# Performance work log

Measured on AMD Instinct MI355X. Metric: run time of the kernel, lower is better.

## Reference

```python
import jax, jax.numpy as jnp
import numpy as np

B, G, C = 16384, 7, 30  # batch, 7x7 grid, 2*5 box params + 20 classes


def setup_inputs() -> dict:
    key = jax.random.key(0)
    k1, k2 = jax.random.split(key)
    pred = jax.random.uniform(k1, (B, G, G, C), dtype=jnp.float32)
    labels = jax.random.uniform(k2, (B, G, G, C), dtype=jnp.float32)
    # channel 0 of labels is the object-presence indicator (==1 where a gt box exists)
    labels = labels.at[..., 0].set((labels[..., 0] > 0.7).astype(jnp.float32))
    return {"pred": pred, "labels": labels}


def _corners(box):
    # box channels: [conf, x, y, w, h]
    x, y, w, h = box[..., 1], box[..., 2], box[..., 3], box[..., 4]
    return x - 0.5 * w, x + 0.5 * w, y - 0.5 * h, y + 0.5 * h  # left,right,top,bottom


def _iou(b1, b2):
    l1, r1, t1, bt1 = _corners(b1)
    l2, r2, t2, bt2 = _corners(b2)
    in_h = jnp.minimum(bt1, bt2) - jnp.maximum(t1, t2)
    in_w = jnp.minimum(r1, r2) - jnp.maximum(l1, l2)
    inter = jnp.where((in_h < 0) | (in_w < 0), 0.0, in_h * in_w)
    area1 = (bt1 - t1) * (r1 - l1)
    area2 = (bt2 - t2) * (r2 - l2)
    return inter / (area1 + area2 - inter)


def reference(pred, labels):
    mask = labels[..., 0]                     # [B,7,7] object indicator (0/1)
    box1 = pred[..., 0:5]
    box2 = pred[..., 5:10]
    gt = labels[..., 0:5]
    iou1 = _iou(box1, gt)
    iou2 = _iou(box2, gt)
    best = iou1 >= iou2                       # responsible box per cell
    sel = jnp.where(best[..., None], box1, box2)
    iou_max = jnp.where(best, iou1, iou2)
    iou_min = jnp.where(best, iou2, iou1)
    center = 5.0 * ((sel[..., 1] - gt[..., 1]) ** 2 + (sel[..., 2] - gt[..., 2]) ** 2)
    wh = 5.0 * ((jnp.sqrt(sel[..., 3]) - jnp.sqrt(gt[..., 3])) ** 2
                + (jnp.sqrt(sel[..., 4]) - jnp.sqrt(gt[..., 4])) ** 2)
    cls = jnp.sum((pred[..., 10:] - labels[..., 10:]) ** 2, axis=-1)

    def msum(x):
        return jnp.sum(x * mask)

    # [center, wh, obj_conf, noobj_conf, classification]
    return jnp.stack([msum(center), msum(wh), msum(iou_max), msum(iou_min), msum(cls)])
```

## Files before the change

kernel.cpp:

```cpp
#include <hip/hip_runtime.h>
#include <stdint.h>

#define NCH   30
#define TPB   256
#define TILE  64
#define TW    (TILE * NCH)
#define TF4   (TW / 4)
#define NBLK  2048

__device__ __forceinline__ float iou_f(float x1, float y1, float w1, float h1,
                                       float x2, float y2, float w2, float h2) {
    float l1 = x1 - 0.5f * w1, r1 = x1 + 0.5f * w1;
    float t1 = y1 - 0.5f * h1, b1 = y1 + 0.5f * h1;
    float l2 = x2 - 0.5f * w2, r2 = x2 + 0.5f * w2;
    float t2 = y2 - 0.5f * h2, b2 = y2 + 0.5f * h2;
    float in_h = fminf(b1, b2) - fmaxf(t1, t2);
    float in_w = fminf(r1, r2) - fmaxf(l1, l2);
    float inter = (in_h < 0.f || in_w < 0.f) ? 0.f : in_h * in_w;
    float a1 = (b1 - t1) * (r1 - l1);
    float a2 = (b2 - t2) * (r2 - l2);
    return inter / (a1 + a2 - inter);
}

__device__ __forceinline__ void cell_loss(const float* __restrict__ pp,
                                          const float* __restrict__ lp,
                                          float& v0, float& v1, float& v2,
                                          float& v3, float& v4) {
    const float2 l01 = *(const float2*)(lp);
    const float mask = l01.x;
    if (mask == 0.f) return;

    const float2 l23 = *(const float2*)(lp + 2);
    const float2 l45 = *(const float2*)(lp + 4);
    const float gx = l01.y, gy = l23.x, gw = l23.y, gh = l45.x;

    const float2 p01 = *(const float2*)(pp);
    const float2 p23 = *(const float2*)(pp + 2);
    const float2 p45 = *(const float2*)(pp + 4);
    const float2 p67 = *(const float2*)(pp + 6);
    const float2 p89 = *(const float2*)(pp + 8);

    const float i1 = iou_f(p01.y, p23.x, p23.y, p45.x, gx, gy, gw, gh);
    const float i2 = iou_f(p67.x, p67.y, p89.x, p89.y, gx, gy, gw, gh);
    const bool best = (i1 >= i2);
    const float sx = best ? p01.y : p67.x;
    const float sy = best ? p23.x : p67.y;
    const float sw = best ? p23.y : p89.x;
    const float sh = best ? p45.x : p89.y;
    const float imax = best ? i1 : i2;
    const float imin = best ? i2 : i1;

    const float center = 5.f * ((sx - gx) * (sx - gx) + (sy - gy) * (sy - gy));
    const float dw = sqrtf(sw) - sqrtf(gw);
    const float dh = sqrtf(sh) - sqrtf(gh);
    const float wh = 5.f * (dw * dw + dh * dh);

    float cls = 0.f;
#pragma unroll
    for (int k = 0; k < 10; ++k) {
        const float2 pd = *(const float2*)(pp + 10 + 2 * k);
        const float2 ld = *(const float2*)(lp + 10 + 2 * k);
        const float dx = pd.x - ld.x;
        const float dy = pd.y - ld.y;
        cls += dx * dx + dy * dy;
    }

    v0 += center * mask;
    v1 += wh * mask;
    v2 += imax * mask;
    v3 += imin * mask;
    v4 += cls * mask;
}

__global__ __launch_bounds__(TPB) void yolo_partial(const float* __restrict__ pred,
                                                    const float* __restrict__ lab,
                                                    float* __restrict__ partial,
                                                    int n_cells) {
    __shared__ float s[2 * TW];
    __shared__ float red[5][TPB / 64];

    const int tid  = threadIdx.x;
    const int wave = tid >> 6;
    const int lane = tid & 63;
    const int bid  = blockIdx.x;
    const int NB   = gridDim.x;
    const int nt   = n_cells / TILE;

    float v0 = 0.f, v1 = 0.f, v2 = 0.f, v3 = 0.f, v4 = 0.f;

    const int i0 = tid, i1 = tid + TPB, i2 = tid + 2 * TPB, i3 = tid + 3 * TPB;

    for (int t = bid; t < nt; t += NB) {
        const size_t gbase = (size_t)t * TW;

        {
            const float4* s0 = (const float4*)((i0 < TF4 ? pred + gbase + (size_t)i0 * 4
                                                         : lab  + gbase + (size_t)(i0 - TF4) * 4));
            const float4* s1 = (const float4*)((i1 < TF4 ? pred + gbase + (size_t)i1 * 4
                                                         : lab  + gbase + (size_t)(i1 - TF4) * 4));
            const float4* s2 = (const float4*)((i2 < TF4 ? pred + gbase + (size_t)i2 * 4
                                                         : lab  + gbase + (size_t)(i2 - TF4) * 4));
            float4 r0 = *s0;
            float4 r1 = *s1;
            float4 r2 = *s2;
            float4 r3;
            if (i3 < 2 * TF4) {
                const float4* s3 = (const float4*)((i3 < TF4 ? pred + gbase + (size_t)i3 * 4
                                                             : lab  + gbase + (size_t)(i3 - TF4) * 4));
                r3 = *s3;
            }
            *(float4*)(s + (size_t)i0 * 4) = r0;
            *(float4*)(s + (size_t)i1 * 4) = r1;
            *(float4*)(s + (size_t)i2 * 4) = r2;
            if (i3 < 2 * TF4) *(float4*)(s + (size_t)i3 * 4) = r3;
        }
        __syncthreads();

        if (tid < TILE) {
            cell_loss(s + tid * NCH, s + TW + tid * NCH, v0, v1, v2, v3, v4);
        }
        __syncthreads();
    }

    const int rem_start = nt * TILE;
    if (bid == 0 && rem_start < n_cells) {
        for (int c = rem_start + tid; c < n_cells; c += TPB) {
            cell_loss(pred + (size_t)c * NCH, lab + (size_t)c * NCH,
                      v0, v1, v2, v3, v4);
        }
    }

#pragma unroll
    for (int off = 32; off > 0; off >>= 1) {
        v0 += __shfl_down(v0, off);
        v1 += __shfl_down(v1, off);
        v2 += __shfl_down(v2, off);
        v3 += __shfl_down(v3, off);
        v4 += __shfl_down(v4, off);
    }
    if (lane == 0) {
        red[0][wave] = v0;
        red[1][wave] = v1;
        red[2][wave] = v2;
        red[3][wave] = v3;
        red[4][wave] = v4;
    }
    __syncthreads();
    if (tid < 5) {
        float sacc = 0.f;
#pragma unroll
        for (int w = 0; w < TPB / 64; ++w) sacc += red[tid][w];
        partial[(size_t)bid * 5 + tid] = sacc;
    }
}

__global__ __launch_bounds__(256) void final_reduce(const float* __restrict__ partial,
                                                    float* __restrict__ out,
                                                    int n_blocks) {
    __shared__ float red[5][4];
    const int tid = threadIdx.x;
    float v0 = 0.f, v1 = 0.f, v2 = 0.f, v3 = 0.f, v4 = 0.f;
    for (int b = tid; b < n_blocks; b += 256) {
        const float* p = partial + (size_t)b * 5;
        v0 += p[0]; v1 += p[1]; v2 += p[2]; v3 += p[3]; v4 += p[4];
    }
#pragma unroll
    for (int off = 32; off > 0; off >>= 1) {
        v0 += __shfl_down(v0, off);
        v1 += __shfl_down(v1, off);
        v2 += __shfl_down(v2, off);
        v3 += __shfl_down(v3, off);
        v4 += __shfl_down(v4, off);
    }
    const int wave = tid >> 6;
    const int lane = tid & 63;
    if (lane == 0) {
        red[0][wave] = v0;
        red[1][wave] = v1;
        red[2][wave] = v2;
        red[3][wave] = v3;
        red[4][wave] = v4;
    }
    __syncthreads();
    if (tid < 5) {
        float sacc = 0.f;
#pragma unroll
        for (int w = 0; w < 4; ++w) sacc += red[tid][w];
        out[tid] = sacc;
    }
}

extern "C" void kernel_launch(void* const* d_in, const int* in_sizes, int n_in,
                              void* d_out, int out_size, void* d_ws, size_t ws_size,
                              hipStream_t stream) {
    const float* pred = (const float*)d_in[0];
    const float* lab  = (const float*)d_in[1];
    float* out = (float*)d_out;
    float* partial = (float*)d_ws;

    const int n_cells = in_sizes[0] / NCH;

    hipLaunchKernelGGL(yolo_partial, dim3(NBLK), dim3(TPB), 0, stream,
                       pred, lab, partial, n_cells);
    hipLaunchKernelGGL(final_reduce, dim3(1), dim3(256), 0, stream,
                       partial, out, NBLK);
}
```

Baseline: 210.8 us.

## Prefetch label tiles and skip loading pred for cells without objects

Labels are now loaded one tile ahead into a double-buffered shared array. A wave ballot over the object-indicator channel builds a 64-bit mask of cells that hold objects, and only the pred float4 chunks that overlap those cells are fetched. Since only about 30% of cells hold an object, this is meant to cut pred traffic from global memory and overlap label loads with compute. The grid size also drops from 2048 to 1536 blocks. In exchange there is an extra ballot pass, extra synchronization and more shared memory, and at DRAM sector granularity the partial pred reads may not save much bandwidth.

```diff
diff --git a/kernel.cpp b/kernel.cpp
--- a/kernel.cpp
+++ b/kernel.cpp
@@ -6,7 +6,7 @@
 #define TILE  64
 #define TW    (TILE * NCH)
 #define TF4   (TW / 4)
-#define NBLK  2048
+#define NBLK  1536
 
 __device__ __forceinline__ float iou_f(float x1, float y1, float w1, float h1,
                                        float x2, float y2, float w2, float h2) {
@@ -76,7 +76,9 @@
                                                     const float* __restrict__ lab,
                                                     float* __restrict__ partial,
                                                     int n_cells) {
-    __shared__ float s[2 * TW];
+    __shared__ float sp[TW];
+    __shared__ float sl[2][TW];
+    __shared__ unsigned long long sbits;
     __shared__ float red[5][TPB / 64];
 
     const int tid  = threadIdx.x;
@@ -86,40 +88,74 @@
     const int NB   = gridDim.x;
     const int nt   = n_cells / TILE;
 
+    const int  idx0 = tid;
+    const int  idx1 = TPB + tid;
+    const bool has1 = (idx1 < TF4);
+
+    const int c00 = (4 * idx0) / NCH, c01 = (4 * idx0 + 3) / NCH;
+    const int c10 = has1 ? (4 * idx1) / NCH : 0;
+    const int c11 = has1 ? (4 * idx1 + 3) / NCH : 0;
+
     float v0 = 0.f, v1 = 0.f, v2 = 0.f, v3 = 0.f, v4 = 0.f;
 
-    const int i0 = tid, i1 = tid + TPB, i2 = tid + 2 * TPB, i3 = tid + 3 * TPB;
-
-    for (int t = bid; t < nt; t += NB) {
-        const size_t gbase = (size_t)t * TW;
-
+    int cur = 0;
+    unsigned long long bits = 0;
+
+    if (bid < nt) {
         {
-            const float4* s0 = (const float4*)((i0 < TF4 ? pred + gbase + (size_t)i0 * 4
-                                                         : lab  + gbase + (size_t)(i0 - TF4) * 4));
-            const float4* s1 = (const float4*)((i1 < TF4 ? pred + gbase + (size_t)i1 * 4
-                                                         : lab  + gbase + (size_t)(i1 - TF4) * 4));
-            const float4* s2 = (const float4*)((i2 < TF4 ? pred + gbase + (size_t)i2 * 4
-                                                         : lab  + gbase + (size_t)(i2 - TF4) * 4));
-            float4 r0 = *s0;
-            float4 r1 = *s1;
-            float4 r2 = *s2;
-            float4 r3;
-            if (i3 < 2 * TF4) {
-                const float4* s3 = (const float4*)((i3 < TF4 ? pred + gbase + (size_t)i3 * 4
-                                                             : lab  + gbase + (size_t)(i3 - TF4) * 4));
-                r3 = *s3;
+            const size_t gbase = (size_t)bid * TW;
+            float4 l0 = *(const float4*)(lab + gbase + (size_t)idx0 * 4);
+            float4 l1;
+            if (has1) l1 = *(const float4*)(lab + gbase + (size_t)idx1 * 4);
+            *(float4*)(&sl[0][idx0 * 4]) = l0;
+            if (has1) *(float4*)(&sl[0][idx1 * 4]) = l1;
+        }
+        __syncthreads();
+        {
+            const unsigned long long b =
+                __ballot(tid < TILE && sl[0][tid * NCH] != 0.f);
+            if (tid == 0) sbits = b;
+        }
+        __syncthreads();
+        bits = sbits;
+
+        for (int t = bid; t < nt; t += NB) {
+            const int  nxt = cur ^ 1;
+            const bool have_next = (t + NB < nt);
+            const size_t gbase = (size_t)t * TW;
+
+            float4 p0, p1, l0, l1;
+            const bool need0 = (((bits >> c00) & 1ull) | ((bits >> c01) & 1ull));
+            const bool need1 = has1 &&
+                               (((bits >> c10) & 1ull) | ((bits >> c11) & 1ull));
+            if (need0) p0 = *(const float4*)(pred + gbase + (size_t)idx0 * 4);
+            if (need1) p1 = *(const float4*)(pred + gbase + (size_t)idx1 * 4);
+            if (have_next) {
+                const size_t nbase = (size_t)(t + NB) * TW;
+                l0 = *(const float4*)(lab + nbase + (size_t)idx0 * 4);
+                if (has1) l1 = *(const float4*)(lab + nbase + (size_t)idx1 * 4);
             }
-            *(float4*)(s + (size_t)i0 * 4) = r0;
-            *(float4*)(s + (size_t)i1 * 4) = r1;
-            *(float4*)(s + (size_t)i2 * 4) = r2;
-            if (i3 < 2 * TF4) *(float4*)(s + (size_t)i3 * 4) = r3;
-        }
-        __syncthreads();
-
-        if (tid < TILE) {
-            cell_loss(s + tid * NCH, s + TW + tid * NCH, v0, v1, v2, v3, v4);
-        }
-        __syncthreads();
+
+            if (need0) *(float4*)(&sp[idx0 * 4]) = p0;
+            if (need1) *(float4*)(&sp[idx1 * 4]) = p1;
+            if (have_next) {
+                *(float4*)(&sl[nxt][idx0 * 4]) = l0;
+                if (has1) *(float4*)(&sl[nxt][idx1 * 4]) = l1;
+            }
+            __syncthreads();
+
+            if (tid < TILE)
+                cell_loss(sp + tid * NCH, &sl[cur][tid * NCH],
+                          v0, v1, v2, v3, v4);
+
+            unsigned long long b = 0;
+            if (have_next)
+                b = __ballot(tid < TILE && sl[nxt][tid * NCH] != 0.f);
+            if (tid == 0) sbits = b;
+            __syncthreads();
+            bits = sbits;
+            cur = nxt;
+        }
     }
 
     const int rem_start = nt * TILE;
```

New measurement: 201.3 us (median of 2 runs). 4.5% less time.
